# Kernel tuning notes

Hardware: AMD Instinct MI355X
Metric: run time of the kernel (lower is better)

The kernel has to match this reference:

```python
import jax, jax.numpy as jnp
import numpy as np

B, N, D, M, H = 16, 2048, 512, 512, 8
DH = D // H
PDE_STEPS = 3
DT = 0.01


def layer_norm(x, g, b, eps=1e-5):
    mu = x.mean(-1, keepdims=True)
    v = ((x - mu) ** 2).mean(-1, keepdims=True)
    return (x - mu) * jax.lax.rsqrt(v + eps) * g + b


def laplacian1d(f):
    # f: [B, M, D]; Neumann boundary via edge padding
    fp = jnp.pad(f, ((0, 0), (1, 1), (0, 0)), mode='edge')
    return fp[:, :-2] - 2.0 * fp[:, 1:-1] + fp[:, 2:]


def diffuse(f, coef, steps=PDE_STEPS, dt=DT):
    # explicit-Euler diffusion PDE evolution, per-channel coefficient
    for _ in range(steps):
        f = f + dt * coef * laplacian1d(f)
    return f


def setup_inputs() -> dict:
    key = jax.random.key(0)
    ks = jax.random.split(key, 10)
    s = 0.02
    return {
        'embeddings': jax.random.normal(ks[0], (B, N, D), dtype=jnp.float32),
        'positions': jax.random.uniform(ks[1], (B, N, 1), dtype=jnp.float32),
        'sigma': jnp.asarray(0.1, dtype=jnp.float32),
        'alpha': s * jax.random.normal(ks[2], (H, H), dtype=jnp.float32),
        'w_int': s * jax.random.normal(ks[3], (D, D), dtype=jnp.float32),
        'b_int': jnp.zeros((D,), dtype=jnp.float32),
        'diff_coef': 0.5 * jnp.ones((D,), dtype=jnp.float32),
        'W1': s * jax.random.normal(ks[4], (D, D), dtype=jnp.float32),
        'b1': jnp.zeros((D,), dtype=jnp.float32),
        'W2': s * jax.random.normal(ks[5], (D, D), dtype=jnp.float32),
        'b2': jnp.zeros((D,), dtype=jnp.float32),
        'evo_coef': 0.5 * jnp.ones((D,), dtype=jnp.float32),
        'ln1_g': jnp.ones((D,), dtype=jnp.float32),
        'ln1_b': jnp.zeros((D,), dtype=jnp.float32),
        'Wout': s * jax.random.normal(ks[6], (D, D), dtype=jnp.float32),
        'bout': jnp.zeros((D,), dtype=jnp.float32),
        'ln2_g': jnp.ones((D,), dtype=jnp.float32),
        'ln2_b': jnp.zeros((D,), dtype=jnp.float32),
    }


def reference(embeddings, positions, sigma, alpha, w_int, b_int, diff_coef,
              W1, b1, W2, b2, evo_coef, ln1_g, ln1_b, Wout, bout, ln2_g, ln2_b):
    # 1) RBF field projection onto uniform 1D grid in [0,1]
    grid = jnp.linspace(0.0, 1.0, M, dtype=embeddings.dtype)  # [M]
    d2 = (grid[None, :, None] - positions[..., 0][:, None, :]) ** 2  # [B,M,N]
    K = jnp.exp(-d2 / (2.0 * sigma ** 2))
    field = jnp.einsum('bmn,bnd->bmd', K, embeddings)  # [B,M,D]
    # 2) multi-head field interference: learned cross-head coupling + proj
    Fh = field.reshape(B, M, H, DH)
    mix = jnp.einsum('hk,bmkd->bmhd', alpha, Fh).reshape(B, M, D)
    field = field + mix @ w_int + b_int
    # 3) field propagation: diffusion PDE steps
    field = diffuse(field, diff_coef)
    # 4) interaction operator: pointwise gated MLP with residual
    field = field + jax.nn.gelu(field @ W1 + b1) @ W2 + b2
    # 5) field evolution: further diffusion PDE steps
    field = diffuse(field, evo_coef)
    # 6) linear field sampling back at token positions
    u = jnp.clip(positions[..., 0], 0.0, 1.0) * (M - 1)  # [B,N]
    i0 = jnp.clip(jnp.floor(u), 0, M - 2).astype(jnp.int32)
    w = (u - i0.astype(u.dtype))[..., None]  # [B,N,1]
    f0 = jnp.take_along_axis(field, i0[:, :, None], axis=1)  # [B,N,D]
    f1 = jnp.take_along_axis(field, (i0 + 1)[:, :, None], axis=1)
    sampled = (1.0 - w) * f0 + w * f1
    # 7) residual + LN, output proj (dropout=eval/identity), residual + LN
    enh = layer_norm(sampled + embeddings, ln1_g, ln1_b)
    out = enh @ Wout + bout
    out = layer_norm(out + enh, ln2_g, ln2_b)
    return out
```

## Files before the change

kernel.cpp:

```cpp
#include <hip/hip_runtime.h>
#include <hip/hip_bf16.h>
#include <math.h>

#define BB 16
#define NN 2048
#define DD 512
#define MM 512

typedef __attribute__((ext_vector_type(8))) short bf16x8;
typedef __attribute__((ext_vector_type(4))) float f32x4;

__device__ __forceinline__ short f2b(float x) {
  union { __hip_bfloat16 h; short s; } u; u.h = __float2bfloat16(x); return u.s;
}
__device__ __forceinline__ float b2f(short s) {
  union { short s2; __hip_bfloat16 h; } u; u.s2 = s; return __bfloat162float(u.h);
}
__device__ __forceinline__ float gelu_f(float x) {
  float x3 = x * x * x;
  return 0.5f * x * (1.0f + tanhf(0.79788456080286536f * (x + 0.044715f * x3)));
}

template<int BM, int BN, int NT, int WR, int WC, int ACT, int RES,
         bool BIAS, bool WB32, bool WB16, bool BATCH>
__global__ __launch_bounds__(NT) void gemm_mfma(
    const short* __restrict__ A, const short* __restrict__ BT,
    const float* __restrict__ bias, const void* __restrict__ res,
    float* __restrict__ C, short* __restrict__ Cb, int K)
{
  constexpr int WAVES = NT / 64;
  constexpr int MF = BM / WR / 16;
  constexpr int NF = BN / WC / 16;
  constexpr int WMT = BM / WR;
  constexpr int WNT = BN / WC;
  constexpr int CHA = BM / 16;
  constexpr int CHB = BN / 16;

  __shared__ short As[BM * 32];
  __shared__ short Bs[BN * 32];

  const int tid = threadIdx.x;
  const int wid = tid >> 6, lane = tid & 63;
  const int lrow = lane & 15, kg = lane >> 4;
  const int wr = (WR == 1) ? 0 : (wid >> 1);
  const int wc = (WR == 1) ? wid : (wid & 1);

  int r0, c0, z;
  if constexpr (BATCH) {
    z = blockIdx.x; r0 = blockIdx.y * BM; c0 = blockIdx.z * BN;
  } else {
    z = 0; r0 = blockIdx.x * BM; c0 = blockIdx.y * BN;
  }
  const size_t zA  = BATCH ? (size_t)z * MM * K : 0;
  const size_t zBT = BATCH ? (size_t)z * DD * K : 0;
  const size_t zC  = BATCH ? (size_t)z * MM * DD : 0;

  f32x4 acc[MF][NF];
  #pragma unroll
  for (int m = 0; m < MF; ++m)
    #pragma unroll
    for (int n = 0; n < NF; ++n) acc[m][n] = (f32x4){0.f, 0.f, 0.f, 0.f};

  for (int kc = 0; kc < K; kc += 32) {
    #pragma unroll
    for (int i = 0; i < CHB / WAVES; ++i) {
      const int ch = wid * (CHB / WAVES) + i;
      const int col = ch * 16 + (lane >> 2);
      const short* gp = BT + zBT + (size_t)(c0 + col) * K + kc + (lane & 3) * 8;
      __builtin_amdgcn_global_load_lds(
          (const __attribute__((address_space(1))) void*)gp,
          (__attribute__((address_space(3))) void*)&Bs[ch * 512], 16, 0, 0);
    }
    if constexpr (CHA >= WAVES) {
      #pragma unroll
      for (int i = 0; i < CHA / WAVES; ++i) {
        const int ch = wid * (CHA / WAVES) + i;
        const int row = ch * 16 + (lane >> 2);
        const short* gp = A + zA + (size_t)(r0 + row) * K + kc + (lane & 3) * 8;
        __builtin_amdgcn_global_load_lds(
            (const __attribute__((address_space(1))) void*)gp,
            (__attribute__((address_space(3))) void*)&As[ch * 512], 16, 0, 0);
      }
    } else {
      if (wid < CHA) {
        const int ch = wid;
        const int row = ch * 16 + (lane >> 2);
        const short* gp = A + zA + (size_t)(r0 + row) * K + kc + (lane & 3) * 8;
        __builtin_amdgcn_global_load_lds(
            (const __attribute__((address_space(1))) void*)gp,
            (__attribute__((address_space(3))) void*)&As[ch * 512], 16, 0, 0);
      }
    }
    __syncthreads();

    bf16x8 af[MF], bfv[NF];
    #pragma unroll
    for (int m = 0; m < MF; ++m)
      af[m] = *(const bf16x8*)&As[(wr * WMT + m * 16 + lrow) * 32 + kg * 8];
    #pragma unroll
    for (int n = 0; n < NF; ++n)
      bfv[n] = *(const bf16x8*)&Bs[(wc * WNT + n * 16 + lrow) * 32 + kg * 8];
    #pragma unroll
    for (int m = 0; m < MF; ++m)
      #pragma unroll
      for (int n = 0; n < NF; ++n)
        acc[m][n] = __builtin_amdgcn_mfma_f32_16x16x32_bf16(af[m], bfv[n], acc[m][n], 0, 0, 0);
    __syncthreads();
  }

  #pragma unroll
  for (int m = 0; m < MF; ++m) {
    #pragma unroll
    for (int n = 0; n < NF; ++n) {
      const int col = c0 + wc * WNT + n * 16 + lrow;
      const int row0 = r0 + wr * WMT + m * 16 + kg * 4;
      float bi = 0.0f;
      if constexpr (BIAS) bi = bias[col];
      #pragma unroll
      for (int r = 0; r < 4; ++r) {
        float x = acc[m][n][r] + bi;
        if constexpr (ACT == 1) x = gelu_f(x);
        const size_t off = zC + (size_t)(row0 + r) * DD + col;
        if constexpr (RES == 1) x += ((const float*)res)[off];
        if constexpr (RES == 2) x += b2f(((const short*)res)[off]);
        if constexpr (WB32) C[off] = x;
        if constexpr (WB16) Cb[off] = f2b(x);
      }
    }
  }
}

__global__ __launch_bounds__(256) void kmat_kernel(
    const float* __restrict__ pos, const float* __restrict__ sigp,
    short* __restrict__ Kmat)
{
  const int gid = blockIdx.x * 256 + threadIdx.x;
  const int n8 = gid & 255;
  const int m  = (gid >> 8) & (MM - 1);
  const int b  = gid >> 17;
  const float s = sigp[0];
  const float inv2s2 = 1.0f / (2.0f * s * s);
  const float g = (float)m * (1.0f / 511.0f);
  const float* pp = pos + (size_t)b * NN + n8 * 8;
  const float4 p0 = *(const float4*)pp;
  const float4 p1 = *(const float4*)(pp + 4);
  const float pv[8] = {p0.x, p0.y, p0.z, p0.w, p1.x, p1.y, p1.z, p1.w};
  bf16x8 o;
  #pragma unroll
  for (int j = 0; j < 8; ++j) {
    const float d = g - pv[j];
    o[j] = f2b(__expf(-(d * d) * inv2s2));
  }
  *(bf16x8*)&Kmat[((size_t)b * MM + m) * NN + n8 * 8] = o;
}

__global__ __launch_bounds__(256) void wtrans_kernel(
    const float* __restrict__ w0, const float* __restrict__ w1,
    const float* __restrict__ w2, const float* __restrict__ w3,
    short* __restrict__ outW)
{
  __shared__ float tle[32][33];
  const int z = blockIdx.z;
  const float* W = (z == 0) ? w0 : (z == 1) ? w1 : (z == 2) ? w2 : w3;
  short* WT = outW + (size_t)z * DD * DD;
  const int bx = blockIdx.x * 32;
  const int by = blockIdx.y * 32;
  const int t = threadIdx.x;
  const int r = t >> 3, c4 = (t & 7) * 4;
  const float4 v = *(const float4*)(W + (size_t)(bx + r) * DD + by + c4);
  tle[r][c4 + 0] = v.x; tle[r][c4 + 1] = v.y; tle[r][c4 + 2] = v.z; tle[r][c4 + 3] = v.w;
  __syncthreads();
  const short4 o = make_short4(f2b(tle[c4 + 0][r]), f2b(tle[c4 + 1][r]),
                               f2b(tle[c4 + 2][r]), f2b(tle[c4 + 3][r]));
  *(short4*)(WT + (size_t)(by + r) * DD + bx + c4) = o;
}

__global__ __launch_bounds__(256) void embtrans_kernel(
    const float* __restrict__ emb, short* __restrict__ embT)
{
  __shared__ float tle[32][33];
  const int z = blockIdx.z;
  const int bx = blockIdx.x * 32;
  const int by = blockIdx.y * 32;
  const int t = threadIdx.x;
  const int r = t >> 3, c4 = (t & 7) * 4;
  const float4 v = *(const float4*)(emb + ((size_t)z * NN + bx + r) * DD + by + c4);
  tle[r][c4 + 0] = v.x; tle[r][c4 + 1] = v.y; tle[r][c4 + 2] = v.z; tle[r][c4 + 3] = v.w;
  __syncthreads();
  const short4 o = make_short4(f2b(tle[c4 + 0][r]), f2b(tle[c4 + 1][r]),
                               f2b(tle[c4 + 2][r]), f2b(tle[c4 + 3][r]));
  *(short4*)(embT + ((size_t)z * DD + by + r) * NN + bx + c4) = o;
}

__global__ __launch_bounds__(256) void mix_kernel(
    const float* __restrict__ field, const float* __restrict__ alpha,
    short* __restrict__ mixout)
{
  __shared__ float row[DD];
  __shared__ float al[64];
  const size_t r = blockIdx.x;
  const int t = threadIdx.x;
  const float* fr = field + r * DD;
  *(float2*)&row[t * 2] = *(const float2*)&fr[t * 2];
  if (t < 64) al[t] = alpha[t];
  __syncthreads();
  const int j = t * 2;
  const int h = j >> 6;
  const int jj = j & 63;
  float s0 = 0.0f, s1 = 0.0f;
  #pragma unroll
  for (int k = 0; k < 8; ++k) {
    const float a = al[h * 8 + k];
    const float2 v = *(const float2*)&row[k * 64 + jj];
    s0 += a * v.x;
    s1 += a * v.y;
  }
  *(short2*)&mixout[r * DD + j] = make_short2(f2b(s0), f2b(s1));
}

__device__ __forceinline__ float4 dstep(float4 fm, float4 f, float4 fp, float4 a) {
  float4 o;
  o.x = f.x + a.x * (fm.x - 2.0f * f.x + fp.x);
  o.y = f.y + a.y * (fm.y - 2.0f * f.y + fp.y);
  o.z = f.z + a.z * (fm.z - 2.0f * f.z + fp.z);
  o.w = f.w + a.w * (fm.w - 2.0f * f.w + fp.w);
  return o;
}

template<bool WB16>
__global__ __launch_bounds__(256) void diffuse3_kernel(
    const float* __restrict__ in, float* __restrict__ out,
    const float* __restrict__ coef, short* __restrict__ bfout)
{
  const size_t base = ((size_t)blockIdx.x * 256 + threadIdx.x) * 4;
  const int d = (int)(base & (DD - 1));
  const int m = (int)((base >> 9) & (MM - 1));
  const size_t rowbase = base - (size_t)m * DD;

  float4 u[7];
  #pragma unroll
  for (int o = 0; o < 7; ++o) {
    int mm = m + o - 3;
    mm = mm < 0 ? 0 : (mm > MM - 1 ? MM - 1 : mm);
    u[o] = *(const float4*)(in + rowbase + (size_t)mm * DD);
  }
  const float4 c = *(const float4*)(coef + d);
  float4 a;
  a.x = 0.01f * c.x; a.y = 0.01f * c.y; a.z = 0.01f * c.z; a.w = 0.01f * c.w;

  float4 v[5];
  #pragma unroll
  for (int o = 0; o < 5; ++o) v[o] = dstep(u[o], u[o + 1], u[o + 2], a);
  float4 w2[3];
  #pragma unroll
  for (int o = 0; o < 3; ++o) w2[o] = dstep(v[o], v[o + 1], v[o + 2], a);
  const float4 r = dstep(w2[0], w2[1], w2[2], a);

  *(float4*)(out + base) = r;
  if constexpr (WB16) {
    *(short4*)(bfout + base) = make_short4(f2b(r.x), f2b(r.y), f2b(r.z), f2b(r.w));
  }
}

__device__ __forceinline__ void ln_stats_512(float sum, float sq, float& mu, float& inv_std) {
  #pragma unroll
  for (int off = 32; off >= 1; off >>= 1) {
    sum += __shfl_down(sum, off);
    sq  += __shfl_down(sq,  off);
  }
  __shared__ float red[8];
  __shared__ float mv[2];
  const int lane = threadIdx.x & 63;
  const int wid = threadIdx.x >> 6;
  if (lane == 0) { red[wid] = sum; red[4 + wid] = sq; }
  __syncthreads();
  if (threadIdx.x == 0) {
    float ts = red[0] + red[1] + red[2] + red[3];
    float tq = red[4] + red[5] + red[6] + red[7];
    float m = ts * (1.0f / 512.0f);
    float v = tq * (1.0f / 512.0f) - m * m;
    mv[0] = m;
    mv[1] = rsqrtf(v + 1e-5f);
  }
  __syncthreads();
  mu = mv[0];
  inv_std = mv[1];
}

__global__ __launch_bounds__(256) void sample_ln_kernel(
    const float* __restrict__ field, const float* __restrict__ pos,
    const float* __restrict__ emb, const float* __restrict__ g,
    const float* __restrict__ be, short* __restrict__ enhb)
{
  const size_t row = blockIdx.x;
  const int b = (int)(row >> 11);
  const int t = threadIdx.x;

  const float p = pos[row];
  const float u = fminf(fmaxf(p, 0.0f), 1.0f) * 511.0f;
  int i0 = (int)floorf(u);
  if (i0 > MM - 2) i0 = MM - 2;
  if (i0 < 0) i0 = 0;
  const float w = u - (float)i0;

  const float* f0 = field + ((size_t)b * MM + i0) * DD;
  const int j = t * 2;
  const float2 a0 = *(const float2*)(f0 + j);
  const float2 a1 = *(const float2*)(f0 + DD + j);
  const float2 e = *(const float2*)(emb + row * DD + j);
  const float sx = (1.0f - w) * a0.x + w * a1.x + e.x;
  const float sy = (1.0f - w) * a0.y + w * a1.y + e.y;

  float mu, is;
  ln_stats_512(sx + sy, sx * sx + sy * sy, mu, is);

  const float2 gg = *(const float2*)(g + j);
  const float2 bb2 = *(const float2*)(be + j);
  *(short2*)&enhb[row * DD + j] = make_short2(
      f2b((sx - mu) * is * gg.x + bb2.x),
      f2b((sy - mu) * is * gg.y + bb2.y));
}

__global__ __launch_bounds__(256) void ln2_kernel(
    float* __restrict__ out, const float* __restrict__ g,
    const float* __restrict__ be)
{
  const size_t row = blockIdx.x;
  const int t = threadIdx.x;
  const int j = t * 2;
  const float2 x = *(const float2*)(out + row * DD + j);
  float mu, is;
  ln_stats_512(x.x + x.y, x.x * x.x + x.y * x.y, mu, is);
  const float2 gg = *(const float2*)(g + j);
  const float2 bb2 = *(const float2*)(be + j);
  float2 o;
  o.x = (x.x - mu) * is * gg.x + bb2.x;
  o.y = (x.y - mu) * is * gg.y + bb2.y;
  *(float2*)(out + row * DD + j) = o;
}


extern "C" void kernel_launch(void* const* d_in, const int* in_sizes, int n_in,
                              void* d_out, int out_size, void* d_ws, size_t ws_size,
                              hipStream_t stream)
{
  const float* emb   = (const float*)d_in[0];
  const float* pos   = (const float*)d_in[1];
  const float* sigma = (const float*)d_in[2];
  const float* alpha = (const float*)d_in[3];
  const float* w_int = (const float*)d_in[4];
  const float* b_int = (const float*)d_in[5];
  const float* diffc = (const float*)d_in[6];
  const float* W1    = (const float*)d_in[7];
  const float* b1    = (const float*)d_in[8];
  const float* W2    = (const float*)d_in[9];
  const float* b2    = (const float*)d_in[10];
  const float* evoc  = (const float*)d_in[11];
  const float* ln1g  = (const float*)d_in[12];
  const float* ln1b  = (const float*)d_in[13];
  const float* Wout  = (const float*)d_in[14];
  const float* bout  = (const float*)d_in[15];
  const float* ln2g  = (const float*)d_in[16];
  const float* ln2b  = (const float*)d_in[17];

  float* out = (float*)d_out;
  char* w = (char*)d_ws;
  float* f0    = (float*)w;
  short* Kmat  = (short*)(w + 16777216);
  float* f1    = (float*)(w + 16777216);
  short* mixb  = (short*)(w + 33554432);
  short* hb    = (short*)(w + 41943040);
  short* embT  = (short*)(w + 50331648);
  short* enhb  = (short*)(w + 50331648);
  short* wT    = (short*)(w + 83886080);
  short* wintT = wT;
  short* w1T   = wT + (size_t)DD * DD;
  short* w2T   = wT + (size_t)2 * DD * DD;
  short* woutT = wT + (size_t)3 * DD * DD;

  const dim3 blk(256);
  const int diff_blocks = BB * MM * DD / 4 / 256;

  wtrans_kernel<<<dim3(16, 16, 4), blk, 0, stream>>>(w_int, W1, W2, Wout, wT);
  embtrans_kernel<<<dim3(64, 16, 16), blk, 0, stream>>>(emb, embT);
  kmat_kernel<<<dim3(BB * MM * NN / 8 / 256), blk, 0, stream>>>(pos, sigma, Kmat);

  gemm_mfma<64, 128, 256, 1, 4, 0, 0, false, true, false, true>
      <<<dim3(BB, MM / 64, DD / 128), blk, 0, stream>>>(
          Kmat, embT, nullptr, nullptr, f0, nullptr, NN);

  mix_kernel<<<dim3(BB * MM), blk, 0, stream>>>(f0, alpha, mixb);
  gemm_mfma<64, 128, 256, 1, 4, 0, 1, true, true, false, false>
      <<<dim3(BB * MM / 64, DD / 128), blk, 0, stream>>>(
          mixb, wintT, b_int, f0, f0, nullptr, DD);

  diffuse3_kernel<true><<<dim3(diff_blocks), blk, 0, stream>>>(f0, f1, diffc, mixb);

  gemm_mfma<64, 128, 256, 1, 4, 1, 0, true, false, true, false>
      <<<dim3(BB * MM / 64, DD / 128), blk, 0, stream>>>(
          mixb, w1T, b1, nullptr, nullptr, hb, DD);
  gemm_mfma<64, 128, 256, 1, 4, 0, 1, true, true, false, false>
      <<<dim3(BB * MM / 64, DD / 128), blk, 0, stream>>>(
          hb, w2T, b2, f1, f1, nullptr, DD);

  diffuse3_kernel<false><<<dim3(diff_blocks), blk, 0, stream>>>(f1, f0, evoc, nullptr);

  sample_ln_kernel<<<dim3(BB * NN), blk, 0, stream>>>(f0, pos, emb, ln1g, ln1b, enhb);

  gemm_mfma<64, 512, 512, 1, 8, 0, 2, true, true, false, false>
      <<<dim3(BB * NN / 64, 1), dim3(512), 0, stream>>>(
          enhb, woutT, bout, enhb, out, nullptr, DD);
  ln2_kernel<<<dim3(BB * NN), blk, 0, stream>>>(out, ln2g, ln2b);
}
```

Baseline: 368.7 us.

## Double-buffer GEMM LDS staging and fuse output projection with final LayerNorm

Makes the MFMA GEMM double-buffer its LDS tiles, so the next K-chunk is fetched while the current one is multiplied, and removes one barrier per iteration. Adds a dedicated output GEMM that applies bias and the second LayerNorm in its epilogue, with a cross-wave reduction of row statistics, which removes the separate ln2 pass and the round trip of the fp32 output through memory. The enh residual is folded into the weight by adding the identity to the diagonal of Wout^T before bf16 conversion. That avoids reading the residual again but rounds (W+I) to bf16, which may cost some precision. Doubling the LDS buffers can also lower occupancy.

```diff
diff --git a/kernel.cpp b/kernel.cpp
--- a/kernel.cpp
+++ b/kernel.cpp
@@ -36,8 +36,8 @@
   constexpr int CHA = BM / 16;
   constexpr int CHB = BN / 16;
 
-  __shared__ short As[BM * 32];
-  __shared__ short Bs[BN * 32];
+  __shared__ short As[2][BM * 32];
+  __shared__ short Bs[2][BN * 32];
 
   const int tid = threadIdx.x;
   const int wid = tid >> 6, lane = tid & 63;
@@ -55,13 +55,7 @@
   const size_t zBT = BATCH ? (size_t)z * DD * K : 0;
   const size_t zC  = BATCH ? (size_t)z * MM * DD : 0;
 
-  f32x4 acc[MF][NF];
-  #pragma unroll
-  for (int m = 0; m < MF; ++m)
-    #pragma unroll
-    for (int n = 0; n < NF; ++n) acc[m][n] = (f32x4){0.f, 0.f, 0.f, 0.f};
-
-  for (int kc = 0; kc < K; kc += 32) {
+  auto stage = [&](int bf, int kc) {
     #pragma unroll
     for (int i = 0; i < CHB / WAVES; ++i) {
       const int ch = wid * (CHB / WAVES) + i;
@@ -69,7 +63,7 @@
       const short* gp = BT + zBT + (size_t)(c0 + col) * K + kc + (lane & 3) * 8;
       __builtin_amdgcn_global_load_lds(
           (const __attribute__((address_space(1))) void*)gp,
-          (__attribute__((address_space(3))) void*)&Bs[ch * 512], 16, 0, 0);
+          (__attribute__((address_space(3))) void*)&Bs[bf][ch * 512], 16, 0, 0);
     }
     if constexpr (CHA >= WAVES) {
       #pragma unroll
@@ -79,33 +73,47 @@
         const short* gp = A + zA + (size_t)(r0 + row) * K + kc + (lane & 3) * 8;
         __builtin_amdgcn_global_load_lds(
             (const __attribute__((address_space(1))) void*)gp,
-            (__attribute__((address_space(3))) void*)&As[ch * 512], 16, 0, 0);
+            (__attribute__((address_space(3))) void*)&As[bf][ch * 512], 16, 0, 0);
       }
     } else {
       if (wid < CHA) {
-        const int ch = wid;
-        const int row = ch * 16 + (lane >> 2);
+        const int row = wid * 16 + (lane >> 2);
         const short* gp = A + zA + (size_t)(r0 + row) * K + kc + (lane & 3) * 8;
         __builtin_amdgcn_global_load_lds(
             (const __attribute__((address_space(1))) void*)gp,
-            (__attribute__((address_space(3))) void*)&As[ch * 512], 16, 0, 0);
+            (__attribute__((address_space(3))) void*)&As[bf][wid * 512], 16, 0, 0);
       }
     }
-    __syncthreads();
+  };
+
+  f32x4 acc[MF][NF];
+  #pragma unroll
+  for (int m = 0; m < MF; ++m)
+    #pragma unroll
+    for (int n = 0; n < NF; ++n) acc[m][n] = (f32x4){0.f, 0.f, 0.f, 0.f};
+
+  stage(0, 0);
+  __syncthreads();
+
+  int buf = 0;
+  for (int kc = 0; kc < K; kc += 32) {
+    if (kc + 32 < K) stage(buf ^ 1, kc + 32);
 
     bf16x8 af[MF], bfv[NF];
     #pragma unroll
     for (int m = 0; m < MF; ++m)
-      af[m] = *(const bf16x8*)&As[(wr * WMT + m * 16 + lrow) * 32 + kg * 8];
+      af[m] = *(const bf16x8*)&As[buf][(wr * WMT + m * 16 + lrow) * 32 + kg * 8];
     #pragma unroll
     for (int n = 0; n < NF; ++n)
-      bfv[n] = *(const bf16x8*)&Bs[(wc * WNT + n * 16 + lrow) * 32 + kg * 8];
+      bfv[n] = *(const bf16x8*)&Bs[buf][(wc * WNT + n * 16 + lrow) * 32 + kg * 8];
     #pragma unroll
     for (int m = 0; m < MF; ++m)
       #pragma unroll
       for (int n = 0; n < NF; ++n)
         acc[m][n] = __builtin_amdgcn_mfma_f32_16x16x32_bf16(af[m], bfv[n], acc[m][n], 0, 0, 0);
+
     __syncthreads();
+    buf ^= 1;
   }
 
   #pragma unroll
@@ -125,6 +133,125 @@
         if constexpr (RES == 2) x += b2f(((const short*)res)[off]);
         if constexpr (WB32) C[off] = x;
         if constexpr (WB16) Cb[off] = f2b(x);
+      }
+    }
+  }
+}
+
+__global__ __launch_bounds__(512) void gemm_out_ln(
+    const short* __restrict__ A, const short* __restrict__ BT,
+    const float* __restrict__ bias, const float* __restrict__ g,
+    const float* __restrict__ be, float* __restrict__ out)
+{
+  constexpr int BM = 64, BN = 512, K = 512;
+  constexpr int WAVES = 8, CHB = BN / 16, CHA = BM / 16;
+
+  __shared__ short As[2][BM * 32];
+  __shared__ short Bs[2][BN * 32];
+  __shared__ float redS[8][64], redQ[8][64];
+  __shared__ float lnMu[64], lnIs[64];
+
+  const int tid = threadIdx.x;
+  const int wid = tid >> 6, lane = tid & 63;
+  const int lrow = lane & 15, kg = lane >> 4;
+  const int wc = wid;
+  const int r0 = blockIdx.x * BM;
+
+  auto stage = [&](int bf, int kc) {
+    #pragma unroll
+    for (int i = 0; i < CHB / WAVES; ++i) {
+      const int ch = wid * (CHB / WAVES) + i;
+      const int col = ch * 16 + (lane >> 2);
+      const short* gp = BT + (size_t)col * K + kc + (lane & 3) * 8;
+      __builtin_amdgcn_global_load_lds(
+          (const __attribute__((address_space(1))) void*)gp,
+          (__attribute__((address_space(3))) void*)&Bs[bf][ch * 512], 16, 0, 0);
+    }
+    if (wid < CHA) {
+      const int row = wid * 16 + (lane >> 2);
+      const short* gp = A + (size_t)(r0 + row) * K + kc + (lane & 3) * 8;
+      __builtin_amdgcn_global_load_lds(
+          (const __attribute__((address_space(1))) void*)gp,
+          (__attribute__((address_space(3))) void*)&As[bf][wid * 512], 16, 0, 0);
+    }
+  };
+
+  f32x4 acc[4][4];
+  #pragma unroll
+  for (int m = 0; m < 4; ++m)
+    #pragma unroll
+    for (int n = 0; n < 4; ++n) acc[m][n] = (f32x4){0.f, 0.f, 0.f, 0.f};
+
+  stage(0, 0);
+  __syncthreads();
+  int buf = 0;
+  for (int kc = 0; kc < K; kc += 32) {
+    if (kc + 32 < K) stage(buf ^ 1, kc + 32);
+    bf16x8 af[4], bfv[4];
+    #pragma unroll
+    for (int m = 0; m < 4; ++m)
+      af[m] = *(const bf16x8*)&As[buf][(m * 16 + lrow) * 32 + kg * 8];
+    #pragma unroll
+    for (int n = 0; n < 4; ++n)
+      bfv[n] = *(const bf16x8*)&Bs[buf][(wc * 64 + n * 16 + lrow) * 32 + kg * 8];
+    #pragma unroll
+    for (int m = 0; m < 4; ++m)
+      #pragma unroll
+      for (int n = 0; n < 4; ++n)
+        acc[m][n] = __builtin_amdgcn_mfma_f32_16x16x32_bf16(af[m], bfv[n], acc[m][n], 0, 0, 0);
+    __syncthreads();
+    buf ^= 1;
+  }
+
+  #pragma unroll
+  for (int m = 0; m < 4; ++m) {
+    #pragma unroll
+    for (int n = 0; n < 4; ++n) {
+      const float bi = bias[wc * 64 + n * 16 + lrow];
+      #pragma unroll
+      for (int r = 0; r < 4; ++r) acc[m][n][r] += bi;
+    }
+  }
+  #pragma unroll
+  for (int m = 0; m < 4; ++m) {
+    #pragma unroll
+    for (int r = 0; r < 4; ++r) {
+      float ps = acc[m][0][r] + acc[m][1][r] + acc[m][2][r] + acc[m][3][r];
+      float pq = acc[m][0][r] * acc[m][0][r] + acc[m][1][r] * acc[m][1][r] +
+                 acc[m][2][r] * acc[m][2][r] + acc[m][3][r] * acc[m][3][r];
+      #pragma unroll
+      for (int off = 8; off >= 1; off >>= 1) {
+        ps += __shfl_xor(ps, off);
+        pq += __shfl_xor(pq, off);
+      }
+      if (lrow == 0) {
+        redS[wid][m * 16 + kg * 4 + r] = ps;
+        redQ[wid][m * 16 + kg * 4 + r] = pq;
+      }
+    }
+  }
+  __syncthreads();
+  if (tid < 64) {
+    float s = 0.f, q = 0.f;
+    #pragma unroll
+    for (int w = 0; w < 8; ++w) { s += redS[w][tid]; q += redQ[w][tid]; }
+    const float mu = s * (1.0f / 512.0f);
+    const float var = q * (1.0f / 512.0f) - mu * mu;
+    lnMu[tid] = mu;
+    lnIs[tid] = rsqrtf(var + 1e-5f);
+  }
+  __syncthreads();
+  #pragma unroll
+  for (int m = 0; m < 4; ++m) {
+    #pragma unroll
+    for (int n = 0; n < 4; ++n) {
+      const int col = wc * 64 + n * 16 + lrow;
+      const float gc = g[col], bc = be[col];
+      #pragma unroll
+      for (int r = 0; r < 4; ++r) {
+        const int row = m * 16 + kg * 4 + r;
+        out[(size_t)(r0 + row) * DD + col] =
+            (acc[m][n][r] - lnMu[row]) * lnIs[row] * gc + bc;
       }
     }
   }
@@ -170,8 +297,13 @@
   const float4 v = *(const float4*)(W + (size_t)(bx + r) * DD + by + c4);
   tle[r][c4 + 0] = v.x; tle[r][c4 + 1] = v.y; tle[r][c4 + 2] = v.z; tle[r][c4 + 3] = v.w;
   __syncthreads();
-  const short4 o = make_short4(f2b(tle[c4 + 0][r]), f2b(tle[c4 + 1][r]),
-                               f2b(tle[c4 + 2][r]), f2b(tle[c4 + 3][r]));
+  short4 o;
+  #pragma unroll
+  for (int j = 0; j < 4; ++j) {
+    float val = tle[c4 + j][r];
+    if (z == 3 && (bx + c4 + j) == (by + r)) val += 1.0f;
+    ((short*)&o)[j] = f2b(val);
+  }
   *(short4*)(WT + (size_t)(by + r) * DD + bx + c4) = o;
 }
 
@@ -319,24 +451,6 @@
   *(short2*)&enhb[row * DD + j] = make_short2(
       f2b((sx - mu) * is * gg.x + bb2.x),
       f2b((sy - mu) * is * gg.y + bb2.y));
-}
-
-__global__ __launch_bounds__(256) void ln2_kernel(
-    float* __restrict__ out, const float* __restrict__ g,
-    const float* __restrict__ be)
-{
-  const size_t row = blockIdx.x;
-  const int t = threadIdx.x;
-  const int j = t * 2;
-  const float2 x = *(const float2*)(out + row * DD + j);
-  float mu, is;
-  ln_stats_512(x.x + x.y, x.x * x.x + x.y * x.y, mu, is);
-  const float2 gg = *(const float2*)(g + j);
-  const float2 bb2 = *(const float2*)(be + j);
-  float2 o;
-  o.x = (x.x - mu) * is * gg.x + bb2.x;
-  o.y = (x.y - mu) * is * gg.y + bb2.y;
-  *(float2*)(out + row * DD + j) = o;
 }
 
 
@@ -407,8 +521,6 @@
 
   sample_ln_kernel<<<dim3(BB * NN), blk, 0, stream>>>(f0, pos, emb, ln1g, ln1b, enhb);
 
-  gemm_mfma<64, 512, 512, 1, 8, 0, 2, true, true, false, false>
-      <<<dim3(BB * NN / 64, 1), dim3(512), 0, stream>>>(
-          enhb, woutT, bout, enhb, out, nullptr, DD);
-  ln2_kernel<<<dim3(BB * NN), blk, 0, stream>>>(out, ln2g, ln2b);
-}
+  gemm_out_ln<<<dim3(BB * NN / 64), dim3(512), 0, stream>>>(
+      enhb, woutT, bout, ln2g, ln2b, out);
+}
```

Measured after the change: 347.9 us. 5.6% less time.
